# Optimization experiments

Hardware: AMD Instinct MI355X
Metric: run time of the kernel (lower is better)

## Reference

```python
import jax, jax.numpy as jnp
import numpy as np

DEG2RAD = np.float32(np.pi / 180.0)


def _rot(theta_deg, axis):
    # pytorch3d RotateAxisAngle uses degrees
    t = theta_deg[0] * DEG2RAD
    c, s = jnp.cos(t), jnp.sin(t)
    one, zero = jnp.ones_like(c), jnp.zeros_like(c)
    if axis == 'X':
        rows = [one, zero, zero, zero, c, -s, zero, s, c]
    elif axis == 'Y':
        rows = [c, zero, s, zero, one, zero, -s, zero, c]
    else:
        rows = [c, -s, zero, s, c, zero, zero, zero, one]
    return jnp.stack(rows).reshape(3, 3)


def _sample(verts, faces, fidx, uv):
    # gather sampled triangles: [N,3,3]
    tri = verts[faces[fidx]]
    v0, v1, v2 = tri[:, 0], tri[:, 1], tri[:, 2]
    # pytorch3d barycentric parametrization: w0=1-sqrt(u), w1=sqrt(u)(1-v), w2=sqrt(u)v
    su = jnp.sqrt(uv[:, 0:1])
    v = uv[:, 1:2]
    pts = (1.0 - su) * v0 + su * (1.0 - v) * v1 + su * v * v2
    n = jnp.cross(v1 - v0, v2 - v0)
    n = n / (jnp.linalg.norm(n, axis=-1, keepdims=True) + 1e-8)
    return pts, n


def _chamfer(x, y, nx, ny):
    # brute-force pairwise squared distances [N,M]
    d2 = (jnp.sum(x * x, -1)[:, None] + jnp.sum(y * y, -1)[None, :]
          - 2.0 * (x @ y.T))
    ixy = jnp.argmin(d2, axis=1)
    iyx = jnp.argmin(d2, axis=0)
    cham_x = jnp.take_along_axis(d2, ixy[:, None], axis=1)[:, 0]
    cham_y = jnp.take_along_axis(d2, iyx[None, :], axis=0)[0, :]
    loss_c = cham_x.mean() + cham_y.mean()
    # normals term: 1 - |cos| at nearest neighbors (pytorch3d abs_cosine=True)
    cos_x = jnp.abs(jnp.sum(nx * ny[ixy], axis=-1))
    cos_y = jnp.abs(jnp.sum(ny * nx[iyx], axis=-1))
    loss_n = (1.0 - cos_x).mean() + (1.0 - cos_y).mean()
    return loss_c + loss_n


def setup_inputs() -> dict:
    key = jax.random.key(0)
    ks = jax.random.split(key, 12)
    V, F, N = 40000, 80000, 10000
    return {
        'verts_mov': jax.random.normal(ks[0], (V, 3), jnp.float32),
        'faces_mov': jax.random.randint(ks[1], (F, 3), 0, V, jnp.int32),
        'verts_fix': jax.random.normal(ks[2], (V, 3), jnp.float32),
        'faces_fix': jax.random.randint(ks[3], (F, 3), 0, V, jnp.int32),
        'translation': jax.random.normal(ks[4], (1, 3), jnp.float32),
        'angle_x': jax.random.normal(ks[5], (1,), jnp.float32),
        'angle_y': jax.random.normal(ks[6], (1,), jnp.float32),
        'angle_z': jax.random.normal(ks[7], (1,), jnp.float32),
        'fidx_mov': jax.random.randint(ks[8], (N,), 0, F, jnp.int32),
        'uv_mov': jax.random.uniform(ks[9], (N, 2), jnp.float32),
        'fidx_fix': jax.random.randint(ks[10], (N,), 0, F, jnp.int32),
        'uv_fix': jax.random.uniform(ks[11], (N, 2), jnp.float32),
    }


def reference(verts_mov, faces_mov, verts_fix, faces_fix, translation,
              angle_x, angle_y, angle_z, fidx_mov, uv_mov, fidx_fix, uv_fix):
    # rigid transform: translate then rotate about X, Y, Z (degrees)
    p = verts_mov + translation
    p = p @ _rot(angle_x, 'X').T
    p = p @ _rot(angle_y, 'Y').T
    p = p @ _rot(angle_z, 'Z').T
    pts_m, n_m = _sample(p, faces_mov, fidx_mov, uv_mov)
    pts_f, n_f = _sample(verts_fix, faces_fix, fidx_fix, uv_fix)
    loss = _chamfer(pts_m, pts_f, n_m, n_f)
    return (loss, p)
```

## Files before the change

### kernel.cpp

```cpp
#include <hip/hip_runtime.h>
#include <math.h>

#define NJ  32
#define CB  256
#define IPT 4

__device__ __forceinline__ void xform(float x, float y, float z,
                                      float tx, float ty, float tz,
                                      float cx, float sx, float cy, float sy,
                                      float cz, float sz,
                                      float& ox, float& oy, float& oz)
{
    x += tx; y += ty; z += tz;
    float x1 = x;
    float y1 = cx*y - sx*z;
    float z1 = sx*y + cx*z;
    float x2 =  cy*x1 + sy*z1;
    float y2 = y1;
    float z2 = -sy*x1 + cy*z1;
    ox = cz*x2 - sz*y2;
    oy = sz*x2 + cz*y2;
    oz = z2;
}

__global__ void k_transform(const float* __restrict__ verts,
                            const float* __restrict__ trans,
                            const float* __restrict__ ax,
                            const float* __restrict__ ay,
                            const float* __restrict__ az,
                            float* __restrict__ out, int V)
{
    int i = blockIdx.x * blockDim.x + threadIdx.x;
    if (i >= V) return;
    const float D2R = 0.017453292519943295f;
    float txr = ax[0]*D2R, tyr = ay[0]*D2R, tzr = az[0]*D2R;
    float cx = cosf(txr), sx = sinf(txr);
    float cy = cosf(tyr), sy = sinf(tyr);
    float cz = cosf(tzr), sz = sinf(tzr);
    float ox, oy, oz;
    xform(verts[3*i+0], verts[3*i+1], verts[3*i+2],
          trans[0], trans[1], trans[2], cx, sx, cy, sy, cz, sz, ox, oy, oz);
    out[3*i+0] = ox; out[3*i+1] = oy; out[3*i+2] = oz;
}

__global__ void k_sample2(const float* __restrict__ vertsM, const int* __restrict__ facesM,
                          const int* __restrict__ fidxM, const float* __restrict__ uvM,
                          float4* __restrict__ ptsM, float4* __restrict__ nrmM,
                          const float* __restrict__ vertsF, const int* __restrict__ facesF,
                          const int* __restrict__ fidxF, const float* __restrict__ uvF,
                          float4* __restrict__ ptsF, float4* __restrict__ nrmF,
                          const float* __restrict__ trans,
                          const float* __restrict__ ax,
                          const float* __restrict__ ay,
                          const float* __restrict__ az, int N)
{
    int which = blockIdx.y;
    const float* verts = which ? vertsF : vertsM;
    const int*   faces = which ? facesF : facesM;
    const int*   fidx  = which ? fidxF  : fidxM;
    const float* uv    = which ? uvF    : uvM;
    float4* ptsS = which ? ptsF : ptsM;
    float4* nrm  = which ? nrmF : nrmM;

    int i = blockIdx.x * blockDim.x + threadIdx.x;
    if (i >= N) return;
    int f  = fidx[i];
    int i0 = faces[3*f+0], i1 = faces[3*f+1], i2 = faces[3*f+2];
    float v0x = verts[3*i0+0], v0y = verts[3*i0+1], v0z = verts[3*i0+2];
    float v1x = verts[3*i1+0], v1y = verts[3*i1+1], v1z = verts[3*i1+2];
    float v2x = verts[3*i2+0], v2y = verts[3*i2+1], v2z = verts[3*i2+2];

    if (!which) {
        const float D2R = 0.017453292519943295f;
        float txr = ax[0]*D2R, tyr = ay[0]*D2R, tzr = az[0]*D2R;
        float cx = cosf(txr), sx = sinf(txr);
        float cy = cosf(tyr), sy = sinf(tyr);
        float cz = cosf(tzr), sz = sinf(tzr);
        xform(v0x, v0y, v0z, trans[0], trans[1], trans[2], cx,sx,cy,sy,cz,sz, v0x,v0y,v0z);
        xform(v1x, v1y, v1z, trans[0], trans[1], trans[2], cx,sx,cy,sy,cz,sz, v1x,v1y,v1z);
        xform(v2x, v2y, v2z, trans[0], trans[1], trans[2], cx,sx,cy,sy,cz,sz, v2x,v2y,v2z);
    }

    float su = sqrtf(uv[2*i+0]);
    float vv = uv[2*i+1];
    float a = 1.0f - su;
    float b = su * (1.0f - vv);
    float c = su * vv;
    float px = a*v0x + b*v1x + c*v2x;
    float py = a*v0y + b*v1y + c*v2y;
    float pz = a*v0z + b*v1z + c*v2z;

    float e1x = v1x - v0x, e1y = v1y - v0y, e1z = v1z - v0z;
    float e2x = v2x - v0x, e2y = v2y - v0y, e2z = v2z - v0z;
    float nx = e1y*e2z - e1z*e2y;
    float ny = e1z*e2x - e1x*e2z;
    float nz = e1x*e2y - e1y*e2x;
    float nn = sqrtf(nx*nx + ny*ny + nz*nz) + 1e-8f;
    nx /= nn; ny /= nn; nz /= nn;

    ptsS[i] = make_float4(px, py, pz, px*px + py*py + pz*pz);
    nrm[i]  = make_float4(nx, ny, nz, 0.0f);
}

__global__ void k_cham2(const float4* __restrict__ Pm, const float4* __restrict__ Pf,
                        float* __restrict__ pval, int* __restrict__ pidx, int N)
{
    int dir = blockIdx.z;
    const float4* X = dir ? Pf : Pm;
    const float4* Y = dir ? Pm : Pf;
    float* pv = pval + (size_t)dir * NJ * N;
    int*   pi = pidx + (size_t)dir * NJ * N;

    __shared__ float4 tile[((10000 + NJ - 1) / NJ) + 8];
    int chunk = blockIdx.y;
    int j0 = (int)(((long long)N * chunk) / NJ);
    int j1 = (int)(((long long)N * (chunk + 1)) / NJ);
    int cnt = j1 - j0;
    for (int t = threadIdx.x; t < cnt; t += CB) tile[t] = Y[j0 + t];
    __syncthreads();

    int ibase = blockIdx.x * CB * IPT + threadIdx.x;

    float xs0[IPT], xs1[IPT], xs2[IPT], xw[IPT];
    #pragma unroll
    for (int p = 0; p < IPT; ++p) {
        int i = ibase + p * CB;
        float4 x = (i < N) ? X[i] : make_float4(0.f, 0.f, 0.f, 0.f);
        xs0[p] = -2.0f * x.x;
        xs1[p] = -2.0f * x.y;
        xs2[p] = -2.0f * x.z;
        xw[p]  = x.w;
    }
    float best[IPT]; int bi[IPT];
    #pragma unroll
    for (int p = 0; p < IPT; ++p) { best[p] = 3.4e38f; bi[p] = j0; }

    #pragma unroll 4
    for (int jj = 0; jj < cnt; ++jj) {
        float4 y = tile[jj];
        #pragma unroll
        for (int p = 0; p < IPT; ++p) {
            float d = fmaf(xs0[p], y.x,
                      fmaf(xs1[p], y.y,
                      fmaf(xs2[p], y.z, y.w)));
            if (d < best[p]) { best[p] = d; bi[p] = j0 + jj; }
        }
    }
    #pragma unroll
    for (int p = 0; p < IPT; ++p) {
        int i = ibase + p * CB;
        if (i < N) {
            pv[(size_t)chunk*N + i] = best[p] + xw[p];
            pi[(size_t)chunk*N + i] = bi[p];
        }
    }
}

__global__ void k_combine(const float* __restrict__ pval, const int* __restrict__ pidx,
                          const float4* __restrict__ n_m, const float4* __restrict__ n_f,
                          float* __restrict__ partial, int N)
{
    int dir = blockIdx.y;
    const float* pv = pval + (size_t)dir * NJ * N;
    const int*   pi = pidx + (size_t)dir * NJ * N;

    int i = blockIdx.x * 256 + threadIdx.x;
    float term = 0.0f;
    if (i < N) {
        float best = pv[i]; int bi = pi[i];
        #pragma unroll
        for (int c = 1; c < NJ; ++c) {
            float v = pv[(size_t)c*N + i];
            if (v < best) { best = v; bi = pi[(size_t)c*N + i]; }
        }
        float4 a = dir ? n_f[i]  : n_m[i];
        float4 b = dir ? n_m[bi] : n_f[bi];
        term = best + 1.0f - fabsf(a.x*b.x + a.y*b.y + a.z*b.z);
    }
    __shared__ float red[256];
    red[threadIdx.x] = term;
    __syncthreads();
    for (int s = 128; s > 0; s >>= 1) {
        if (threadIdx.x < s) red[threadIdx.x] += red[threadIdx.x + s];
        __syncthreads();
    }
    if (threadIdx.x == 0) partial[dir * gridDim.x + blockIdx.x] = red[0];
}

__global__ void k_final(const float* __restrict__ partial, int nPart,
                        float* __restrict__ out, int N)
{
    __shared__ float red[256];
    float acc = 0.0f;
    for (int i = threadIdx.x; i < nPart; i += 256) acc += partial[i];
    red[threadIdx.x] = acc;
    __syncthreads();
    for (int s = 128; s > 0; s >>= 1) {
        if (threadIdx.x < s) red[threadIdx.x] += red[threadIdx.x + s];
        __syncthreads();
    }
    if (threadIdx.x == 0) out[0] = red[0] / (float)N;
}

extern "C" void kernel_launch(void* const* d_in, const int* in_sizes, int n_in,
                              void* d_out, int out_size, void* d_ws, size_t ws_size,
                              hipStream_t stream)
{
    const float* verts_mov = (const float*)d_in[0];
    const int*   faces_mov = (const int*)  d_in[1];
    const float* verts_fix = (const float*)d_in[2];
    const int*   faces_fix = (const int*)  d_in[3];
    const float* trans     = (const float*)d_in[4];
    const float* ax        = (const float*)d_in[5];
    const float* ay        = (const float*)d_in[6];
    const float* az        = (const float*)d_in[7];
    const int*   fidx_mov  = (const int*)  d_in[8];
    const float* uv_mov    = (const float*)d_in[9];
    const int*   fidx_fix  = (const int*)  d_in[10];
    const float* uv_fix    = (const float*)d_in[11];

    int V = in_sizes[0] / 3;
    int N = in_sizes[8];

    float* out = (float*)d_out;
    float* p   = out + 1;

    float*  ws      = (float*)d_ws;
    float4* ptsS_m  = (float4*)(ws + 0*4*N);
    float4* n_m     = (float4*)(ws + 1*4*N);
    float4* ptsS_f  = (float4*)(ws + 2*4*N);
    float4* n_f     = (float4*)(ws + 3*4*N);
    float*  pval    = ws + 16*N;
    int*    pidx    = (int*)(ws + 16*N + 2*NJ*N);
    float*  partial = ws + 16*N + 4*NJ*N;

    k_transform<<<(V + 255)/256, 256, 0, stream>>>(verts_mov, trans, ax, ay, az, p, V);

    dim3 gs((N + 255)/256, 2);
    k_sample2<<<gs, 256, 0, stream>>>(verts_mov, faces_mov, fidx_mov, uv_mov, ptsS_m, n_m,
                                      verts_fix, faces_fix, fidx_fix, uv_fix, ptsS_f, n_f,
                                      trans, ax, ay, az, N);

    dim3 gc((N + CB*IPT - 1)/(CB*IPT), NJ, 2);
    k_cham2<<<gc, CB, 0, stream>>>(ptsS_m, ptsS_f, pval, pidx, N);

    int GX = (N + 255)/256;
    dim3 gk(GX, 2);
    k_combine<<<gk, 256, 0, stream>>>(pval, pidx, n_m, n_f, partial, N);

    k_final<<<1, 256, 0, stream>>>(partial, 2*GX, out, N);
}
```

Before: 127.2 us.

## Merge transform and sampling kernels, double chamfer chunks, pack value-index pairs

Fuses the vertex transform and both surface-sampling passes into one launch by partitioning the block index range, removing a kernel launch. Doubles the number of Y-chunks in the chamfer kernel so more blocks run at once on the GPU, and stores each partial min value with its index as a packed float2 so the combine pass does one 8-byte load per chunk. The cost is twice as many partials for the combine kernel to reduce, plus more partial-buffer traffic.

```diff
diff --git a/kernel.cpp b/kernel.cpp
--- a/kernel.cpp
+++ b/kernel.cpp
@@ -1,7 +1,7 @@
 #include <hip/hip_runtime.h>
 #include <math.h>
 
-#define NJ  32
+#define NJ  64
 #define CB  256
 #define IPT 4
 
@@ -23,38 +23,42 @@
     oz = z2;
 }
 
-__global__ void k_transform(const float* __restrict__ verts,
-                            const float* __restrict__ trans,
-                            const float* __restrict__ ax,
-                            const float* __restrict__ ay,
-                            const float* __restrict__ az,
-                            float* __restrict__ out, int V)
-{
-    int i = blockIdx.x * blockDim.x + threadIdx.x;
-    if (i >= V) return;
+__global__ void k_prep(const float* __restrict__ vertsM, const int* __restrict__ facesM,
+                       const int* __restrict__ fidxM, const float* __restrict__ uvM,
+                       float4* __restrict__ ptsM, float4* __restrict__ nrmM,
+                       const float* __restrict__ vertsF, const int* __restrict__ facesF,
+                       const int* __restrict__ fidxF, const float* __restrict__ uvF,
+                       float4* __restrict__ ptsF, float4* __restrict__ nrmF,
+                       const float* __restrict__ trans,
+                       const float* __restrict__ ax,
+                       const float* __restrict__ ay,
+                       const float* __restrict__ az,
+                       float* __restrict__ pOut,
+                       int V, int N, int nbT, int nbS)
+{
     const float D2R = 0.017453292519943295f;
-    float txr = ax[0]*D2R, tyr = ay[0]*D2R, tzr = az[0]*D2R;
-    float cx = cosf(txr), sx = sinf(txr);
-    float cy = cosf(tyr), sy = sinf(tyr);
-    float cz = cosf(tzr), sz = sinf(tzr);
-    float ox, oy, oz;
-    xform(verts[3*i+0], verts[3*i+1], verts[3*i+2],
-          trans[0], trans[1], trans[2], cx, sx, cy, sy, cz, sz, ox, oy, oz);
-    out[3*i+0] = ox; out[3*i+1] = oy; out[3*i+2] = oz;
-}
-
-__global__ void k_sample2(const float* __restrict__ vertsM, const int* __restrict__ facesM,
-                          const int* __restrict__ fidxM, const float* __restrict__ uvM,
-                          float4* __restrict__ ptsM, float4* __restrict__ nrmM,
-                          const float* __restrict__ vertsF, const int* __restrict__ facesF,
-                          const int* __restrict__ fidxF, const float* __restrict__ uvF,
-                          float4* __restrict__ ptsF, float4* __restrict__ nrmF,
-                          const float* __restrict__ trans,
-                          const float* __restrict__ ax,
-                          const float* __restrict__ ay,
-                          const float* __restrict__ az, int N)
-{
-    int which = blockIdx.y;
+    int b = blockIdx.x;
+
+    if (b < nbT) {
+        int i = b * blockDim.x + threadIdx.x;
+        if (i >= V) return;
+        float txr = ax[0]*D2R, tyr = ay[0]*D2R, tzr = az[0]*D2R;
+        float cx = cosf(txr), sx = sinf(txr);
+        float cy = cosf(tyr), sy = sinf(tyr);
+        float cz = cosf(tzr), sz = sinf(tzr);
+        float ox, oy, oz;
+        xform(vertsM[3*i+0], vertsM[3*i+1], vertsM[3*i+2],
+              trans[0], trans[1], trans[2], cx, sx, cy, sy, cz, sz, ox, oy, oz);
+        pOut[3*i+0] = ox; pOut[3*i+1] = oy; pOut[3*i+2] = oz;
+        return;
+    }
+
+    int bb = b - nbT;
+    int which = (bb >= nbS) ? 1 : 0;
+    int bx = which ? bb - nbS : bb;
+    int i = bx * blockDim.x + threadIdx.x;
+    if (i >= N) return;
+
     const float* verts = which ? vertsF : vertsM;
     const int*   faces = which ? facesF : facesM;
     const int*   fidx  = which ? fidxF  : fidxM;
@@ -62,8 +66,6 @@
     float4* ptsS = which ? ptsF : ptsM;
     float4* nrm  = which ? nrmF : nrmM;
 
-    int i = blockIdx.x * blockDim.x + threadIdx.x;
-    if (i >= N) return;
     int f  = fidx[i];
     int i0 = faces[3*f+0], i1 = faces[3*f+1], i2 = faces[3*f+2];
     float v0x = verts[3*i0+0], v0y = verts[3*i0+1], v0z = verts[3*i0+2];
@@ -71,24 +73,23 @@
     float v2x = verts[3*i2+0], v2y = verts[3*i2+1], v2z = verts[3*i2+2];
 
     if (!which) {
-        const float D2R = 0.017453292519943295f;
         float txr = ax[0]*D2R, tyr = ay[0]*D2R, tzr = az[0]*D2R;
         float cx = cosf(txr), sx = sinf(txr);
         float cy = cosf(tyr), sy = sinf(tyr);
         float cz = cosf(tzr), sz = sinf(tzr);
-        xform(v0x, v0y, v0z, trans[0], trans[1], trans[2], cx,sx,cy,sy,cz,sz, v0x,v0y,v0z);
-        xform(v1x, v1y, v1z, trans[0], trans[1], trans[2], cx,sx,cy,sy,cz,sz, v1x,v1y,v1z);
-        xform(v2x, v2y, v2z, trans[0], trans[1], trans[2], cx,sx,cy,sy,cz,sz, v2x,v2y,v2z);
+        xform(v0x,v0y,v0z, trans[0],trans[1],trans[2], cx,sx,cy,sy,cz,sz, v0x,v0y,v0z);
+        xform(v1x,v1y,v1z, trans[0],trans[1],trans[2], cx,sx,cy,sy,cz,sz, v1x,v1y,v1z);
+        xform(v2x,v2y,v2z, trans[0],trans[1],trans[2], cx,sx,cy,sy,cz,sz, v2x,v2y,v2z);
     }
 
     float su = sqrtf(uv[2*i+0]);
     float vv = uv[2*i+1];
     float a = 1.0f - su;
-    float b = su * (1.0f - vv);
+    float bq = su * (1.0f - vv);
     float c = su * vv;
-    float px = a*v0x + b*v1x + c*v2x;
-    float py = a*v0y + b*v1y + c*v2y;
-    float pz = a*v0z + b*v1z + c*v2z;
+    float px = a*v0x + bq*v1x + c*v2x;
+    float py = a*v0y + bq*v1y + c*v2y;
+    float pz = a*v0z + bq*v1z + c*v2z;
 
     float e1x = v1x - v0x, e1y = v1y - v0y, e1z = v1z - v0z;
     float e2x = v2x - v0x, e2y = v2y - v0y, e2z = v2z - v0z;
@@ -103,13 +104,12 @@
 }
 
 __global__ void k_cham2(const float4* __restrict__ Pm, const float4* __restrict__ Pf,
-                        float* __restrict__ pval, int* __restrict__ pidx, int N)
+                        float2* __restrict__ pvi, int N)
 {
     int dir = blockIdx.z;
     const float4* X = dir ? Pf : Pm;
     const float4* Y = dir ? Pm : Pf;
-    float* pv = pval + (size_t)dir * NJ * N;
-    int*   pi = pidx + (size_t)dir * NJ * N;
+    float2* out = pvi + (size_t)dir * NJ * N;
 
     __shared__ float4 tile[((10000 + NJ - 1) / NJ) + 8];
     int chunk = blockIdx.y;
@@ -149,29 +149,28 @@
     #pragma unroll
     for (int p = 0; p < IPT; ++p) {
         int i = ibase + p * CB;
-        if (i < N) {
-            pv[(size_t)chunk*N + i] = best[p] + xw[p];
-            pi[(size_t)chunk*N + i] = bi[p];
-        }
-    }
-}
-
-__global__ void k_combine(const float* __restrict__ pval, const int* __restrict__ pidx,
+        if (i < N)
+            out[(size_t)chunk*N + i] = make_float2(best[p] + xw[p],
+                                                   __int_as_float(bi[p]));
+    }
+}
+
+__global__ void k_combine(const float2* __restrict__ pvi,
                           const float4* __restrict__ n_m, const float4* __restrict__ n_f,
                           float* __restrict__ partial, int N)
 {
     int dir = blockIdx.y;
-    const float* pv = pval + (size_t)dir * NJ * N;
-    const int*   pi = pidx + (size_t)dir * NJ * N;
+    const float2* base = pvi + (size_t)dir * NJ * N;
 
     int i = blockIdx.x * 256 + threadIdx.x;
     float term = 0.0f;
     if (i < N) {
-        float best = pv[i]; int bi = pi[i];
+        float2 v0 = base[i];
+        float best = v0.x; int bi = __float_as_int(v0.y);
         #pragma unroll
         for (int c = 1; c < NJ; ++c) {
-            float v = pv[(size_t)c*N + i];
-            if (v < best) { best = v; bi = pi[(size_t)c*N + i]; }
+            float2 v = base[(size_t)c*N + i];
+            if (v.x < best) { best = v.x; bi = __float_as_int(v.y); }
         }
         float4 a = dir ? n_f[i]  : n_m[i];
         float4 b = dir ? n_m[bi] : n_f[bi];
@@ -230,23 +229,23 @@
     float4* n_m     = (float4*)(ws + 1*4*N);
     float4* ptsS_f  = (float4*)(ws + 2*4*N);
     float4* n_f     = (float4*)(ws + 3*4*N);
-    float*  pval    = ws + 16*N;
-    int*    pidx    = (int*)(ws + 16*N + 2*NJ*N);
+    float2* pvi     = (float2*)(ws + 16*N);
     float*  partial = ws + 16*N + 4*NJ*N;
 
-    k_transform<<<(V + 255)/256, 256, 0, stream>>>(verts_mov, trans, ax, ay, az, p, V);
-
-    dim3 gs((N + 255)/256, 2);
-    k_sample2<<<gs, 256, 0, stream>>>(verts_mov, faces_mov, fidx_mov, uv_mov, ptsS_m, n_m,
-                                      verts_fix, faces_fix, fidx_fix, uv_fix, ptsS_f, n_f,
-                                      trans, ax, ay, az, N);
+    int nbT = (V + 255) / 256;
+    int nbS = (N + 255) / 256;
+    k_prep<<<nbT + 2*nbS, 256, 0, stream>>>(verts_mov, faces_mov, fidx_mov, uv_mov,
+                                            ptsS_m, n_m,
+                                            verts_fix, faces_fix, fidx_fix, uv_fix,
+                                            ptsS_f, n_f,
+                                            trans, ax, ay, az, p, V, N, nbT, nbS);
 
     dim3 gc((N + CB*IPT - 1)/(CB*IPT), NJ, 2);
-    k_cham2<<<gc, CB, 0, stream>>>(ptsS_m, ptsS_f, pval, pidx, N);
+    k_cham2<<<gc, CB, 0, stream>>>(ptsS_m, ptsS_f, pvi, N);
 
     int GX = (N + 255)/256;
     dim3 gk(GX, 2);
-    k_combine<<<gk, 256, 0, stream>>>(pval, pidx, n_m, n_f, partial, N);
+    k_combine<<<gk, 256, 0, stream>>>(pvi, n_m, n_f, partial, N);
 
     k_final<<<1, 256, 0, stream>>>(partial, 2*GX, out, N);
 }
```

Measured after the change: 119.8 us. 1.06x faster.
